# Kernel tuning notes

Hardware: AMD Instinct MI355X
Metric: run time of the kernel (lower is better)

The kernel has to match this reference:

```python
import jax, jax.numpy as jnp
import numpy as np

D_MODEL = 1024
N_HEADS = 16
HEAD_DIM = D_MODEL // N_HEADS
ROPE_THETA = 10000.0
EPS = 1e-6


def _split_qkv(qkv, h):
    b, n, _ = qkv.shape
    qkv = qkv.reshape(b, n, 3, h, -1)          # b n three h d
    qkv = jnp.transpose(qkv, (2, 0, 3, 1, 4))  # three b h n d
    return qkv[0], qkv[1], qkv[2]


def _rms_norm(x, scale):
    # RMSNorm over head dim with learnable per-dim scale (QKNorm)
    var = jnp.mean(jnp.square(x), axis=-1, keepdims=True)
    return x * jax.lax.rsqrt(var + EPS) * scale


def _rope(x, pos):
    # x: [b, h, n, d], pos: [n] float; rotate-half RoPE
    d = x.shape[-1]
    inv_freq = 1.0 / (ROPE_THETA ** (jnp.arange(0, d, 2, dtype=jnp.float32) / d))
    ang = pos[:, None] * inv_freq[None, :]                 # [n, d/2]
    cos = jnp.cos(ang)[None, None]                          # [1,1,n,d/2]
    sin = jnp.sin(ang)[None, None]
    x1 = x[..., 0::2]
    x2 = x[..., 1::2]
    r1 = x1 * cos - x2 * sin
    r2 = x1 * sin + x2 * cos
    return jnp.stack([r1, r2], axis=-1).reshape(x.shape)


def setup_inputs() -> dict:
    key = jax.random.key(0)
    ks = jax.random.split(key, 16)
    d = D_MODEL
    s = 0.02
    inp = {
        "x_1": jax.random.normal(ks[0], (2, 1536, d), dtype=jnp.float32),
        "x_2": jax.random.normal(ks[1], (2, 512, d), dtype=jnp.float32),
        "W_qkv1": jax.random.normal(ks[2], (3 * d, d), dtype=jnp.float32) * s,
        "b_qkv1": jnp.zeros((3 * d,), dtype=jnp.float32),
        "W_qkv2": jax.random.normal(ks[3], (3 * d, d), dtype=jnp.float32) * s,
        "b_qkv2": jnp.zeros((3 * d,), dtype=jnp.float32),
        "W_out1": jax.random.normal(ks[4], (d, d), dtype=jnp.float32) * s,
        "b_out1": jnp.zeros((d,), dtype=jnp.float32),
        "W_out2": jax.random.normal(ks[5], (d, d), dtype=jnp.float32) * s,
        "b_out2": jnp.zeros((d,), dtype=jnp.float32),
        "q_scale1": jnp.ones((HEAD_DIM,), dtype=jnp.float32),
        "k_scale1": jnp.ones((HEAD_DIM,), dtype=jnp.float32),
        "q_scale2": jnp.ones((HEAD_DIM,), dtype=jnp.float32),
        "k_scale2": jnp.ones((HEAD_DIM,), dtype=jnp.float32),
    }
    return inp


def reference(x_1, x_2, W_qkv1, b_qkv1, W_qkv2, b_qkv2,
              W_out1, b_out1, W_out2, b_out2,
              q_scale1, k_scale1, q_scale2, k_scale2):
    b, n1, d = x_1.shape
    n2 = x_2.shape[1]
    h = N_HEADS

    q1, k1, v1 = _split_qkv(x_1 @ W_qkv1.T + b_qkv1, h)
    q2, k2, v2 = _split_qkv(x_2 @ W_qkv2.T + b_qkv2, h)

    q1 = _rms_norm(q1, q_scale1); k1 = _rms_norm(k1, k_scale1)
    q2 = _rms_norm(q2, q_scale2); k2 = _rms_norm(k2, k_scale2)

    # AVRoPE: stream-1 tokens at positions [0, n1), stream-2 continues at [n1, n1+n2)
    pos1 = jnp.arange(n1, dtype=jnp.float32)
    pos2 = n1 + jnp.arange(n2, dtype=jnp.float32)
    q1 = _rope(q1, pos1); q2 = _rope(q2, pos2)
    k1 = _rope(k1, pos1); k2 = _rope(k2, pos2)

    q = jnp.concatenate([q1, q2], axis=-2)   # [b,h,N,dh]
    k = jnp.concatenate([k1, k2], axis=-2)
    v = jnp.concatenate([v1, v2], axis=-2)

    scale = 1.0 / jnp.sqrt(jnp.asarray(q.shape[-1], dtype=q.dtype))
    scores = jnp.einsum('bhqd,bhkd->bhqk', q, k) * scale
    attn = jax.nn.softmax(scores, axis=-1)
    x = jnp.einsum('bhqk,bhkd->bhqd', attn, v)      # [b,h,N,dh]

    x = jnp.transpose(x, (0, 2, 1, 3)).reshape(b, n1 + n2, d)  # merge heads

    out1 = x[:, :n1] @ W_out1.T + b_out1
    out2 = x[:, n1:] @ W_out2.T + b_out2
    return out1, out2
```

## Files before the change

### kernel.cpp

```cpp
#include <hip/hip_runtime.h>
#include <hip/hip_bf16.h>
#include <math.h>

#define D_MODEL 1024
#define N_HEADS 16
#define HEAD_DIM 64
#define SEQ1 1536
#define SEQ2 512
#define NTOT 2048
#define BATCH 2

typedef __attribute__((ext_vector_type(8))) short bf16x8;
typedef __attribute__((ext_vector_type(4))) float f32x4;

__device__ __forceinline__ unsigned short f2bf(float f) {
  unsigned u = __builtin_bit_cast(unsigned, f);
  u += 0x7FFFu + ((u >> 16) & 1u);
  return (unsigned short)(u >> 16);
}
__device__ __forceinline__ float bf2f(unsigned short h) {
  unsigned u = ((unsigned)h) << 16;
  return __builtin_bit_cast(float, u);
}

__device__ __forceinline__ void gload16(const void* g, void* l) {
  __builtin_amdgcn_global_load_lds(
      (const __attribute__((address_space(1))) void*)g,
      (__attribute__((address_space(3))) void*)l, 16, 0, 0);
}

struct CvtArgs {
  const float* src[6];
  unsigned short* dst[6];
  int prefix[7];
};

__global__ __launch_bounds__(256) void cvt_all(CvtArgs a)
{
  int e = (blockIdx.x * 256 + threadIdx.x) * 4;
  if (e >= a.prefix[6]) return;
  int s = 0;
#pragma unroll
  for (int i = 1; i < 6; ++i) s += (e >= a.prefix[i]) ? 1 : 0;
  int lo = e - a.prefix[s];
  float4 v = *(const float4*)(a.src[s] + lo);
  ushort4 o;
  o.x = f2bf(v.x); o.y = f2bf(v.y); o.z = f2bf(v.z); o.w = f2bf(v.w);
  *(ushort4*)(a.dst[s] + lo) = o;
}

struct GemmSeg {
  const unsigned short* A;
  const unsigned short* W;
  const float* bias;
  void* C;
  int N, K, tilesX;
};

template <int WRITE_BF16>
__global__ __launch_bounds__(256) void gemm2(GemmSeg g0, GemmSeg g1, int tiles0)
{
  __shared__ __align__(16) unsigned short Alds[128 * 64];
  __shared__ __align__(16) unsigned short Blds[128 * 64];
  const int id = blockIdx.x;
  const bool in1 = (id >= tiles0);
  const unsigned short* A = in1 ? g1.A : g0.A;
  const unsigned short* W = in1 ? g1.W : g0.W;
  const float* bias = in1 ? g1.bias : g0.bias;
  void* Cv = in1 ? g1.C : g0.C;
  const int N = in1 ? g1.N : g0.N;
  const int K = in1 ? g1.K : g0.K;
  const int tilesX = in1 ? g1.tilesX : g0.tilesX;
  const int lid = in1 ? id - tiles0 : id;
  const int m0 = (lid / tilesX) * 128, n0 = (lid % tilesX) * 128;

  const int tid = threadIdx.x;
  const int lane = tid & 63, wave = tid >> 6;
  const int wm = wave >> 1, wn = wave & 1;
  const int l15 = lane & 15, l4 = lane >> 4;

  f32x4 acc[4][4];
#pragma unroll
  for (int m = 0; m < 4; ++m)
#pragma unroll
    for (int n = 0; n < 4; ++n)
#pragma unroll
      for (int r = 0; r < 4; ++r) acc[m][n][r] = 0.0f;

  for (int k0 = 0; k0 < K; k0 += 64) {
    __syncthreads();
#pragma unroll
    for (int c = 0; c < 4; ++c) {
      int off = c * 4096 + tid * 16;
      int row = off >> 7;
      int c16g = ((off & 127) >> 4) ^ (row & 7);
      int dstb = c * 4096 + (tid >> 6) * 1024;
      gload16(A + (size_t)(m0 + row) * K + k0 + c16g * 8, (char*)Alds + dstb);
      gload16(W + (size_t)(n0 + row) * K + k0 + c16g * 8, (char*)Blds + dstb);
    }
    __syncthreads();
#pragma unroll
    for (int kk = 0; kk < 2; ++kk) {
      bf16x8 af[4], bfr[4];
#pragma unroll
      for (int m = 0; m < 4; ++m) {
        int r = wm * 64 + m * 16 + l15;
        int colb = (kk * 64 + l4 * 16) ^ ((r & 7) << 4);
        af[m] = *(const bf16x8*)((const char*)Alds + r * 128 + colb);
      }
#pragma unroll
      for (int n = 0; n < 4; ++n) {
        int r = wn * 64 + n * 16 + l15;
        int colb = (kk * 64 + l4 * 16) ^ ((r & 7) << 4);
        bfr[n] = *(const bf16x8*)((const char*)Blds + r * 128 + colb);
      }
#pragma unroll
      for (int m = 0; m < 4; ++m)
#pragma unroll
        for (int n = 0; n < 4; ++n)
          acc[m][n] = __builtin_amdgcn_mfma_f32_16x16x32_bf16(
              af[m], bfr[n], acc[m][n], 0, 0, 0);
    }
  }

#pragma unroll
  for (int m = 0; m < 4; ++m)
#pragma unroll
    for (int n = 0; n < 4; ++n)
#pragma unroll
      for (int r = 0; r < 4; ++r) {
        int row = m0 + wm * 64 + m * 16 + l4 * 4 + r;
        int col = n0 + wn * 64 + n * 16 + l15;
        float v = acc[m][n][r] + bias[col];
        if (WRITE_BF16)
          ((unsigned short*)Cv)[(size_t)row * N + col] = f2bf(v);
        else
          ((float*)Cv)[(size_t)row * N + col] = v;
      }
}

__global__ __launch_bounds__(256) void qkv_transform(
    const unsigned short* __restrict__ qkv1,
    const unsigned short* __restrict__ qkv2,
    const float* __restrict__ qs1, const float* __restrict__ ks1,
    const float* __restrict__ qs2, const float* __restrict__ ks2,
    unsigned short* __restrict__ qO, unsigned short* __restrict__ kO,
    unsigned short* __restrict__ vO)
{
  const int row = blockIdx.x;
  const int lane = threadIdx.x & 63;
  const int wave = threadIdx.x >> 6;
  const float QSCALE = 0.18033688011112042f;

  const unsigned short* src;
  const float* qs;
  const float* ks;
  int b, pos;
  if (row < BATCH * SEQ1) {
    b = row / SEQ1;
    pos = row % SEQ1;
    src = qkv1 + (size_t)row * (3 * D_MODEL);
    qs = qs1; ks = ks1;
  } else {
    int r2 = row - BATCH * SEQ1;
    b = r2 / SEQ2;
    pos = SEQ1 + (r2 % SEQ2);
    src = qkv2 + (size_t)r2 * (3 * D_MODEL);
    qs = qs2; ks = ks2;
  }

  const int j = lane >> 1;
  const float LOG2_THETA = 13.287712379549449f;
  float inv_freq = exp2f(-((float)(2 * j) / 64.0f) * LOG2_THETA);
  float ang = (float)pos * inv_freq;
  float sn, cs;
  sincosf(ang, &sn, &cs);

  for (int h = wave; h < N_HEADS; h += 4) {
    float xq = bf2f(src[0 * D_MODEL + h * HEAD_DIM + lane]);
    float xk = bf2f(src[1 * D_MODEL + h * HEAD_DIM + lane]);
    float xv = bf2f(src[2 * D_MODEL + h * HEAD_DIM + lane]);

    float sq = xq * xq, sk = xk * xk;
#pragma unroll
    for (int o = 32; o > 0; o >>= 1) {
      sq += __shfl_xor(sq, o);
      sk += __shfl_xor(sk, o);
    }
    float xqn = xq * rsqrtf(sq * (1.0f / 64.0f) + 1e-6f) * qs[lane];
    float xkn = xk * rsqrtf(sk * (1.0f / 64.0f) + 1e-6f) * ks[lane];

    float pq = __shfl_xor(xqn, 1);
    float pk = __shfl_xor(xkn, 1);
    float oq, ok;
    if (lane & 1) { oq = pq * sn + xqn * cs; ok = pk * sn + xkn * cs; }
    else          { oq = xqn * cs - pq * sn; ok = xkn * cs - pk * sn; }

    size_t o = (((size_t)b * N_HEADS + h) * NTOT + pos) * HEAD_DIM + lane;
    qO[o] = f2bf(oq * QSCALE);
    kO[o] = f2bf(ok);
    vO[o] = f2bf(xv);
  }
}

__global__ __launch_bounds__(256) void v_transpose(
    const unsigned short* __restrict__ v, unsigned short* __restrict__ vt)
{
  const int pt = blockIdx.x, bh = blockIdx.y;
  __shared__ unsigned short t[64][72];
  const int tid = threadIdx.x;
  const unsigned short* src = v + ((size_t)bh * NTOT + pt * 64) * 64;
#pragma unroll
  for (int c = 0; c < 2; ++c) {
    int off = c * 4096 + tid * 16;
    int row = off >> 7, c16 = (off & 127) >> 4;
    bf16x8 x = *(const bf16x8*)(src + row * 64 + c16 * 8);
#pragma unroll
    for (int j = 0; j < 8; ++j) t[row][c16 * 8 + j] = (unsigned short)x[j];
  }
  __syncthreads();
  unsigned short* dst = vt + (size_t)bh * 64 * NTOT + pt * 64;
#pragma unroll
  for (int c = 0; c < 2; ++c) {
    int off = c * 4096 + tid * 16;
    int d = off >> 7, p16 = (off & 127) >> 4;
    bf16x8 x;
#pragma unroll
    for (int j = 0; j < 8; ++j) x[j] = (short)t[p16 * 8 + j][d];
    *(bf16x8*)(dst + (size_t)d * NTOT + p16 * 8) = x;
  }
}

__global__ __launch_bounds__(256) void attn_mfma(
    const unsigned short* __restrict__ Qg, const unsigned short* __restrict__ Kg,
    const unsigned short* __restrict__ VTg,
    unsigned short* __restrict__ xb1, unsigned short* __restrict__ xb2)
{
  const int qt = blockIdx.x, bh = blockIdx.y;
  const int b = bh >> 4, h = bh & 15;
  const int tid = threadIdx.x, lane = tid & 63, w = tid >> 6;
  const int l15 = lane & 15, l4 = lane >> 4;

  __shared__ __align__(16) unsigned short Klds[2][64 * 64];
  __shared__ __align__(16) unsigned short Vlds[2][64 * 64];
  __shared__ __align__(16) unsigned short Plds[64 * 64];

  const size_t base = (size_t)bh * NTOT * HEAD_DIM;
  bf16x8 qf[2];
  {
    const unsigned short* qp =
        Qg + base + (size_t)(qt * 64 + w * 16 + l15) * 64 + l4 * 8;
    qf[0] = *(const bf16x8*)qp;
    qf[1] = *(const bf16x8*)(qp + 32);
  }

  f32x4 acc_o[4];
#pragma unroll
  for (int dt = 0; dt < 4; ++dt)
#pragma unroll
    for (int r = 0; r < 4; ++r) acc_o[dt][r] = 0.0f;
  float m_run = -1e30f, l_run = 0.0f;

  const unsigned short* kp = Kg + base;
  const unsigned short* vtp = VTg + (size_t)bh * HEAD_DIM * NTOT;

#define STAGE(bf, kt)                                                         \
  {                                                                           \
    _Pragma("unroll")                                                         \
    for (int c = 0; c < 2; ++c) {                                             \
      int off = c * 4096 + tid * 16;                                          \
      int row = off >> 7;                                                     \
      int c16g = ((off & 127) >> 4) ^ (row & 7);                              \
      int dstb = c * 4096 + (tid >> 6) * 1024;                                \
      gload16(kp + (size_t)((kt) * 64 + row) * 64 + c16g * 8,                 \
              (char*)Klds[bf] + dstb);                                        \
      gload16(vtp + (size_t)row * NTOT + (kt) * 64 + c16g * 8,                \
              (char*)Vlds[bf] + dstb);                                        \
    }                                                                         \
  }

  STAGE(0, 0);

  for (int kt = 0; kt < NTOT / 64; ++kt) {
    const int cur = kt & 1;
    __syncthreads();
    if (kt + 1 < NTOT / 64) STAGE(cur ^ 1, kt + 1);

    f32x4 sacc[4];
#pragma unroll
    for (int ct = 0; ct < 4; ++ct)
#pragma unroll
      for (int r = 0; r < 4; ++r) sacc[ct][r] = 0.0f;
    __builtin_amdgcn_s_setprio(1);
#pragma unroll
    for (int kk = 0; kk < 2; ++kk) {
#pragma unroll
      for (int ct = 0; ct < 4; ++ct) {
        int r = ct * 16 + l15;
        int colb = (kk * 64 + l4 * 16) ^ ((r & 7) << 4);
        bf16x8 kf = *(const bf16x8*)((const char*)Klds[cur] + r * 128 + colb);
        sacc[ct] = __builtin_amdgcn_mfma_f32_16x16x32_bf16(
            kf, qf[kk], sacc[ct], 0, 0, 0);
      }
    }
    __builtin_amdgcn_s_setprio(0);

    {
      float tm = fmaxf(fmaxf(sacc[0][0], sacc[0][1]),
                       fmaxf(sacc[0][2], sacc[0][3]));
#pragma unroll
      for (int ct = 1; ct < 4; ++ct)
        tm = fmaxf(tm, fmaxf(fmaxf(sacc[ct][0], sacc[ct][1]),
                             fmaxf(sacc[ct][2], sacc[ct][3])));
      tm = fmaxf(tm, __shfl_xor(tm, 16));
      tm = fmaxf(tm, __shfl_xor(tm, 32));
      float mo = m_run;
      if (!__all(tm <= mo + 8.0f)) {
        float mn = fmaxf(mo, tm);
        float fac = exp2f(mo - mn);
        m_run = mn;
        l_run *= fac;
#pragma unroll
        for (int r = 0; r < 4; ++r) {
          float fr = __shfl(fac, l4 * 4 + r);
#pragma unroll
          for (int dt = 0; dt < 4; ++dt) acc_o[dt][r] *= fr;
        }
      }
      float mc = m_run;
      float rs = 0.0f;
      int qrow = w * 16 + l15;
#pragma unroll
      for (int ct = 0; ct < 4; ++ct) {
        float p0 = exp2f(sacc[ct][0] - mc);
        float p1 = exp2f(sacc[ct][1] - mc);
        float p2 = exp2f(sacc[ct][2] - mc);
        float p3 = exp2f(sacc[ct][3] - mc);
        rs += (p0 + p1) + (p2 + p3);
        uint2 pw;
        pw.x = (unsigned)f2bf(p0) | ((unsigned)f2bf(p1) << 16);
        pw.y = (unsigned)f2bf(p2) | ((unsigned)f2bf(p3) << 16);
        *(uint2*)((char*)Plds + qrow * 128 +
                  ((ct * 32 + l4 * 8) ^ ((qrow & 7) << 4))) = pw;
      }
      rs += __shfl_xor(rs, 16);
      rs += __shfl_xor(rs, 32);
      l_run += rs;
    }

    __builtin_amdgcn_s_setprio(1);
#pragma unroll
    for (int ks = 0; ks < 2; ++ks) {
      int pr = w * 16 + l15;
      int pcolb = (ks * 64 + l4 * 16) ^ ((pr & 7) << 4);
      bf16x8 pf = *(const bf16x8*)((const char*)Plds + pr * 128 + pcolb);
#pragma unroll
      for (int dt = 0; dt < 4; ++dt) {
        int vr = dt * 16 + l15;
        int vcolb = (ks * 64 + l4 * 16) ^ ((vr & 7) << 4);
        bf16x8 vf = *(const bf16x8*)((const char*)Vlds[cur] + vr * 128 + vcolb);
        acc_o[dt] = __builtin_amdgcn_mfma_f32_16x16x32_bf16(
            pf, vf, acc_o[dt], 0, 0, 0);
      }
    }
    __builtin_amdgcn_s_setprio(0);
  }
#undef STAGE

  {
    float inv = 1.0f / l_run;
#pragma unroll
    for (int r = 0; r < 4; ++r) {
      float ir = __shfl(inv, l4 * 4 + r);
      int n = qt * 64 + w * 16 + l4 * 4 + r;
      unsigned short* dst;
      if (n < SEQ1) dst = xb1 + ((size_t)b * SEQ1 + n) * D_MODEL;
      else          dst = xb2 + ((size_t)b * SEQ2 + (n - SEQ1)) * D_MODEL;
#pragma unroll
      for (int dt = 0; dt < 4; ++dt)
        dst[h * 64 + dt * 16 + l15] = f2bf(acc_o[dt][r] * ir);
    }
  }
}

extern "C" void kernel_launch(void* const* d_in, const int* in_sizes, int n_in,
                              void* d_out, int out_size, void* d_ws,
                              size_t ws_size, hipStream_t stream)
{
  (void)in_sizes; (void)n_in; (void)out_size; (void)ws_size;

  const float* x1  = (const float*)d_in[0];
  const float* x2  = (const float*)d_in[1];
  const float* Wq1 = (const float*)d_in[2];
  const float* bq1 = (const float*)d_in[3];
  const float* Wq2 = (const float*)d_in[4];
  const float* bq2 = (const float*)d_in[5];
  const float* Wo1 = (const float*)d_in[6];
  const float* bo1 = (const float*)d_in[7];
  const float* Wo2 = (const float*)d_in[8];
  const float* bo2 = (const float*)d_in[9];
  const float* qs1 = (const float*)d_in[10];
  const float* ks1 = (const float*)d_in[11];
  const float* qs2 = (const float*)d_in[12];
  const float* ks2 = (const float*)d_in[13];
  float* out = (float*)d_out;

  unsigned short* ws = (unsigned short*)d_ws;
  const size_t SX1 = (size_t)BATCH * SEQ1 * D_MODEL;
  const size_t SX2 = (size_t)BATCH * SEQ2 * D_MODEL;
  const size_t SW  = (size_t)3 * D_MODEL * D_MODEL;
  const size_t SWO = (size_t)D_MODEL * D_MODEL;
  const size_t SQ1 = (size_t)BATCH * SEQ1 * 3 * D_MODEL;
  const size_t SQ2 = (size_t)BATCH * SEQ2 * 3 * D_MODEL;
  const size_t SH  = (size_t)BATCH * N_HEADS * NTOT * HEAD_DIM;

  unsigned short* x1b  = ws;
  unsigned short* x2b  = x1b + SX1;
  unsigned short* Wq1b = x2b + SX2;
  unsigned short* Wq2b = Wq1b + SW;
  unsigned short* Wo1b = Wq2b + SW;
  unsigned short* Wo2b = Wo1b + SWO;
  unsigned short* qkv1 = Wo2b + SWO;
  unsigned short* qkv2 = qkv1 + SQ1;
  unsigned short* qb   = qkv2 + SQ2;
  unsigned short* kb   = qb + SH;
  unsigned short* vb   = kb + SH;
  unsigned short* vtb  = vb + SH;
  unsigned short* xb1  = vtb + SH;
  unsigned short* xb2  = xb1 + SX1;

  CvtArgs ca;
  ca.src[0] = x1;  ca.dst[0] = x1b;
  ca.src[1] = x2;  ca.dst[1] = x2b;
  ca.src[2] = Wq1; ca.dst[2] = Wq1b;
  ca.src[3] = Wq2; ca.dst[3] = Wq2b;
  ca.src[4] = Wo1; ca.dst[4] = Wo1b;
  ca.src[5] = Wo2; ca.dst[5] = Wo2b;
  ca.prefix[0] = 0;
  ca.prefix[1] = (int)SX1;
  ca.prefix[2] = (int)(SX1 + SX2);
  ca.prefix[3] = (int)(SX1 + SX2 + SW);
  ca.prefix[4] = (int)(SX1 + SX2 + 2 * SW);
  ca.prefix[5] = (int)(SX1 + SX2 + 2 * SW + SWO);
  ca.prefix[6] = (int)(SX1 + SX2 + 2 * SW + 2 * SWO);
  cvt_all<<<(ca.prefix[6] / 4 + 255) / 256, 256, 0, stream>>>(ca);

  {
    GemmSeg s0{x1b, Wq1b, bq1, qkv1, 3 * D_MODEL, D_MODEL, 3 * D_MODEL / 128};
    GemmSeg s1{x2b, Wq2b, bq2, qkv2, 3 * D_MODEL, D_MODEL, 3 * D_MODEL / 128};
    int t0 = (BATCH * SEQ1 / 128) * (3 * D_MODEL / 128);
    int t1 = (BATCH * SEQ2 / 128) * (3 * D_MODEL / 128);
    gemm2<1><<<t0 + t1, 256, 0, stream>>>(s0, s1, t0);
  }

  qkv_transform<<<BATCH * (SEQ1 + SEQ2), 256, 0, stream>>>(
      qkv1, qkv2, qs1, ks1, qs2, ks2, qb, kb, vb);

  v_transpose<<<dim3(NTOT / 64, BATCH * N_HEADS), 256, 0, stream>>>(vb, vtb);

  attn_mfma<<<dim3(NTOT / 64, BATCH * N_HEADS), 256, 0, stream>>>(
      qb, kb, vtb, xb1, xb2);

  {
    GemmSeg s0{xb1, Wo1b, bo1, out, D_MODEL, D_MODEL, D_MODEL / 128};
    GemmSeg s1{xb2, Wo2b, bo2, out + (size_t)BATCH * SEQ1 * D_MODEL,
               D_MODEL, D_MODEL, D_MODEL / 128};
    int t0 = (BATCH * SEQ1 / 128) * (D_MODEL / 128);
    int t1 = (BATCH * SEQ2 / 128) * (D_MODEL / 128);
    gemm2<0><<<t0 + t1, 256, 0, stream>>>(s0, s1, t0);
  }
}
```

Before: 287.5 us.

## Switch attention to 32x32x16 MFMA with register-resident P and 128-row query tiles

Result: no change. 288.2 us (+0.2%).

```diff
diff --git a/kernel.cpp b/kernel.cpp
--- a/kernel.cpp
+++ b/kernel.cpp
@@ -12,6 +12,7 @@
 
 typedef __attribute__((ext_vector_type(8))) short bf16x8;
 typedef __attribute__((ext_vector_type(4))) float f32x4;
+typedef __attribute__((ext_vector_type(16))) float f32x16;
 
 __device__ __forceinline__ unsigned short f2bf(float f) {
   unsigned u = __builtin_bit_cast(unsigned, f);
@@ -21,6 +22,9 @@
 __device__ __forceinline__ float bf2f(unsigned short h) {
   unsigned u = ((unsigned)h) << 16;
   return __builtin_bit_cast(float, u);
+}
+__device__ __forceinline__ unsigned packbf(float a, float b) {
+  return (unsigned)f2bf(a) | ((unsigned)f2bf(b) << 16);
 }
 
 __device__ __forceinline__ void gload16(const void* g, void* l) {
@@ -237,28 +241,28 @@
     unsigned short* __restrict__ xb1, unsigned short* __restrict__ xb2)
 {
   const int qt = blockIdx.x, bh = blockIdx.y;
-  const int b = bh >> 4, h = bh & 15;
+  const int b = bh >> 4, head = bh & 15;
   const int tid = threadIdx.x, lane = tid & 63, w = tid >> 6;
-  const int l15 = lane & 15, l4 = lane >> 4;
+  const int ql = lane & 31, hf = lane >> 5;
 
   __shared__ __align__(16) unsigned short Klds[2][64 * 64];
   __shared__ __align__(16) unsigned short Vlds[2][64 * 64];
-  __shared__ __align__(16) unsigned short Plds[64 * 64];
 
   const size_t base = (size_t)bh * NTOT * HEAD_DIM;
-  bf16x8 qf[2];
+
+  bf16x8 qf[4];
   {
     const unsigned short* qp =
-        Qg + base + (size_t)(qt * 64 + w * 16 + l15) * 64 + l4 * 8;
-    qf[0] = *(const bf16x8*)qp;
-    qf[1] = *(const bf16x8*)(qp + 32);
-  }
-
-  f32x4 acc_o[4];
-#pragma unroll
-  for (int dt = 0; dt < 4; ++dt)
-#pragma unroll
-    for (int r = 0; r < 4; ++r) acc_o[dt][r] = 0.0f;
+        Qg + base + (size_t)(qt * 128 + w * 32 + ql) * 64 + hf * 8;
+#pragma unroll
+    for (int s = 0; s < 4; ++s) qf[s] = *(const bf16x8*)(qp + s * 16);
+  }
+
+  f32x16 acc_o[2];
+#pragma unroll
+  for (int dt = 0; dt < 2; ++dt)
+#pragma unroll
+    for (int r = 0; r < 16; ++r) acc_o[dt][r] = 0.0f;
   float m_run = -1e30f, l_run = 0.0f;
 
   const unsigned short* kp = Kg + base;
@@ -286,81 +290,99 @@
     __syncthreads();
     if (kt + 1 < NTOT / 64) STAGE(cur ^ 1, kt + 1);
 
-    f32x4 sacc[4];
-#pragma unroll
-    for (int ct = 0; ct < 4; ++ct)
-#pragma unroll
-      for (int r = 0; r < 4; ++r) sacc[ct][r] = 0.0f;
+    f32x16 sacc[2];
+#pragma unroll
+    for (int t = 0; t < 2; ++t)
+#pragma unroll
+      for (int r = 0; r < 16; ++r) sacc[t][r] = 0.0f;
     __builtin_amdgcn_s_setprio(1);
 #pragma unroll
-    for (int kk = 0; kk < 2; ++kk) {
-#pragma unroll
-      for (int ct = 0; ct < 4; ++ct) {
-        int r = ct * 16 + l15;
-        int colb = (kk * 64 + l4 * 16) ^ ((r & 7) << 4);
-        bf16x8 kf = *(const bf16x8*)((const char*)Klds[cur] + r * 128 + colb);
-        sacc[ct] = __builtin_amdgcn_mfma_f32_16x16x32_bf16(
-            kf, qf[kk], sacc[ct], 0, 0, 0);
+    for (int t = 0; t < 2; ++t) {
+#pragma unroll
+      for (int s = 0; s < 4; ++s) {
+        int row = t * 32 + ql;
+        int colb = (s * 32 + hf * 16) ^ ((row & 7) << 4);
+        bf16x8 kf = *(const bf16x8*)((const char*)Klds[cur] + row * 128 + colb);
+        sacc[t] = __builtin_amdgcn_mfma_f32_32x32x16_bf16(
+            kf, qf[s], sacc[t], 0, 0, 0);
       }
     }
     __builtin_amdgcn_s_setprio(0);
 
+    float tm = sacc[0][0];
+#pragma unroll
+    for (int t = 0; t < 2; ++t)
+#pragma unroll
+      for (int r = 0; r < 16; ++r) tm = fmaxf(tm, sacc[t][r]);
+    tm = fmaxf(tm, __shfl_xor(tm, 32));
+    if (!__all(tm <= m_run + 8.0f)) {
+      float mn = fmaxf(m_run, tm);
+      float fac = exp2f(m_run - mn);
+      m_run = mn;
+      l_run *= fac;
+#pragma unroll
+      for (int dt = 0; dt < 2; ++dt)
+#pragma unroll
+        for (int r = 0; r < 16; ++r) acc_o[dt][r] *= fac;
+    }
+    const float mc = m_run;
+
+    unsigned c0[8], c1[8];
+    float rs = 0.0f;
     {
-      float tm = fmaxf(fmaxf(sacc[0][0], sacc[0][1]),
-                       fmaxf(sacc[0][2], sacc[0][3]));
-#pragma unroll
-      for (int ct = 1; ct < 4; ++ct)
-        tm = fmaxf(tm, fmaxf(fmaxf(sacc[ct][0], sacc[ct][1]),
-                             fmaxf(sacc[ct][2], sacc[ct][3])));
-      tm = fmaxf(tm, __shfl_xor(tm, 16));
-      tm = fmaxf(tm, __shfl_xor(tm, 32));
-      float mo = m_run;
-      if (!__all(tm <= mo + 8.0f)) {
-        float mn = fmaxf(mo, tm);
-        float fac = exp2f(mo - mn);
-        m_run = mn;
-        l_run *= fac;
-#pragma unroll
-        for (int r = 0; r < 4; ++r) {
-          float fr = __shfl(fac, l4 * 4 + r);
-#pragma unroll
-          for (int dt = 0; dt < 4; ++dt) acc_o[dt][r] *= fr;
-        }
-      }
-      float mc = m_run;
-      float rs = 0.0f;
-      int qrow = w * 16 + l15;
-#pragma unroll
-      for (int ct = 0; ct < 4; ++ct) {
-        float p0 = exp2f(sacc[ct][0] - mc);
-        float p1 = exp2f(sacc[ct][1] - mc);
-        float p2 = exp2f(sacc[ct][2] - mc);
-        float p3 = exp2f(sacc[ct][3] - mc);
-        rs += (p0 + p1) + (p2 + p3);
-        uint2 pw;
-        pw.x = (unsigned)f2bf(p0) | ((unsigned)f2bf(p1) << 16);
-        pw.y = (unsigned)f2bf(p2) | ((unsigned)f2bf(p3) << 16);
-        *(uint2*)((char*)Plds + qrow * 128 +
-                  ((ct * 32 + l4 * 8) ^ ((qrow & 7) << 4))) = pw;
-      }
-      rs += __shfl_xor(rs, 16);
-      rs += __shfl_xor(rs, 32);
-      l_run += rs;
-    }
+      float p0[16], p1[16];
+#pragma unroll
+      for (int r = 0; r < 16; ++r) {
+        p0[r] = exp2f(sacc[0][r] - mc);
+        p1[r] = exp2f(sacc[1][r] - mc);
+        rs += p0[r] + p1[r];
+      }
+#pragma unroll
+      for (int a = 0; a < 4; ++a) {
+        c0[2 * a + 0] = packbf(p0[4 * a + 0], p0[4 * a + 1]);
+        c0[2 * a + 1] = packbf(p0[4 * a + 2], p0[4 * a + 3]);
+        c1[2 * a + 0] = packbf(p1[4 * a + 0], p1[4 * a + 1]);
+        c1[2 * a + 1] = packbf(p1[4 * a + 2], p1[4 * a + 3]);
+      }
+    }
+    rs += __shfl_xor(rs, 32);
+    l_run += rs;
+
+    unsigned r0[4], r1[4];
+    r0[0] = __shfl_xor(hf ? c0[0] : c0[2], 32);
+    r0[1] = __shfl_xor(hf ? c0[1] : c0[3], 32);
+    r0[2] = __shfl_xor(hf ? c0[4] : c0[6], 32);
+    r0[3] = __shfl_xor(hf ? c0[5] : c0[7], 32);
+    r1[0] = __shfl_xor(hf ? c1[0] : c1[2], 32);
+    r1[1] = __shfl_xor(hf ? c1[1] : c1[3], 32);
+    r1[2] = __shfl_xor(hf ? c1[4] : c1[6], 32);
+    r1[3] = __shfl_xor(hf ? c1[5] : c1[7], 32);
 
     __builtin_amdgcn_s_setprio(1);
 #pragma unroll
-    for (int ks = 0; ks < 2; ++ks) {
-      int pr = w * 16 + l15;
-      int pcolb = (ks * 64 + l4 * 16) ^ ((pr & 7) << 4);
-      bf16x8 pf = *(const bf16x8*)((const char*)Plds + pr * 128 + pcolb);
-#pragma unroll
-      for (int dt = 0; dt < 4; ++dt) {
-        int vr = dt * 16 + l15;
-        int vcolb = (ks * 64 + l4 * 16) ^ ((vr & 7) << 4);
-        bf16x8 vf = *(const bf16x8*)((const char*)Vlds[cur] + vr * 128 + vcolb);
-        acc_o[dt] = __builtin_amdgcn_mfma_f32_16x16x32_bf16(
-            pf, vf, acc_o[dt], 0, 0, 0);
+    for (int s = 0; s < 4; ++s) {
+      uint4 pw;
+      const unsigned* cc = (s < 2) ? c0 : c1;
+      const unsigned* rr = (s < 2) ? r0 : r1;
+      if ((s & 1) == 0) {
+        pw.x = hf ? rr[0] : cc[0];
+        pw.y = hf ? rr[1] : cc[1];
+        pw.z = hf ? cc[2] : rr[0];
+        pw.w = hf ? cc[3] : rr[1];
+      } else {
+        pw.x = hf ? rr[2] : cc[4];
+        pw.y = hf ? rr[3] : cc[5];
+        pw.z = hf ? cc[6] : rr[2];
+        pw.w = hf ? cc[7] : rr[3];
+      }
+      bf16x8 pfrag = __builtin_bit_cast(bf16x8, pw);
+#pragma unroll
+      for (int dt = 0; dt < 2; ++dt) {
+        int row = dt * 32 + ql;
+        int colb = (s * 32 + hf * 16) ^ ((row & 7) << 4);
+        bf16x8 vf = *(const bf16x8*)((const char*)Vlds[cur] + row * 128 + colb);
+        acc_o[dt] = __builtin_amdgcn_mfma_f32_32x32x16_bf16(
+            vf, pfrag, acc_o[dt], 0, 0, 0);
       }
     }
     __builtin_amdgcn_s_setprio(0);
@@ -369,17 +391,21 @@
 
   {
     float inv = 1.0f / l_run;
-#pragma unroll
-    for (int r = 0; r < 4; ++r) {
-      float ir = __shfl(inv, l4 * 4 + r);
-      int n = qt * 64 + w * 16 + l4 * 4 + r;
-      unsigned short* dst;
-      if (n < SEQ1) dst = xb1 + ((size_t)b * SEQ1 + n) * D_MODEL;
-      else          dst = xb2 + ((size_t)b * SEQ2 + (n - SEQ1)) * D_MODEL;
-#pragma unroll
-      for (int dt = 0; dt < 4; ++dt)
-        dst[h * 64 + dt * 16 + l15] = f2bf(acc_o[dt][r] * ir);
-    }
+    int n = qt * 128 + w * 32 + ql;
+    unsigned short* dst;
+    if (n < SEQ1) dst = xb1 + ((size_t)b * SEQ1 + n) * D_MODEL;
+    else          dst = xb2 + ((size_t)b * SEQ2 + (n - SEQ1)) * D_MODEL;
+#pragma unroll
+    for (int dt = 0; dt < 2; ++dt)
+#pragma unroll
+      for (int rq = 0; rq < 4; ++rq) {
+        ushort4 o;
+        o.x = f2bf(acc_o[dt][rq * 4 + 0] * inv);
+        o.y = f2bf(acc_o[dt][rq * 4 + 1] * inv);
+        o.z = f2bf(acc_o[dt][rq * 4 + 2] * inv);
+        o.w = f2bf(acc_o[dt][rq * 4 + 3] * inv);
+        *(ushort4*)(dst + head * 64 + dt * 32 + rq * 8 + hf * 4) = o;
+      }
   }
 }
 
@@ -458,7 +484,7 @@
 
   v_transpose<<<dim3(NTOT / 64, BATCH * N_HEADS), 256, 0, stream>>>(vb, vtb);
 
-  attn_mfma<<<dim3(NTOT / 64, BATCH * N_HEADS), 256, 0, stream>>>(
+  attn_mfma<<<dim3(NTOT / 128, BATCH * N_HEADS), 256, 0, stream>>>(
       qb, kb, vtb, xb1, xb2);
 
   {
```
